# Optimization experiments

Hardware: AMD Instinct MI355X
Metric: run time of the kernel (lower is better)

Reference implementation:

```python
import jax, jax.numpy as jnp
import numpy as np

NUM_HEAD = 16
NUM_SEQ = 2048
NUM_FEAT = 1024
HEAD_DIM = NUM_FEAT // NUM_HEAD
LN_EPS = 1e-5


def _constants():
    # decay per head: log(1 - 2^{-5-h})
    decay = jnp.log(1.0 - 2.0 ** (-5.0 - jnp.arange(NUM_HEAD, dtype=jnp.float32)))
    idx = jnp.arange(NUM_SEQ, dtype=jnp.float32)
    diff = idx[:, None] - idx[None, :]                      # [s, s]
    # exp(diff * decay) on lower triangle (incl. diagonal), 0 above
    mask = jnp.where(diff[None] >= 0, jnp.exp(diff[None] * decay[:, None, None]), 0.0)  # [h, s, s]
    # rotary angles: each frequency repeated twice
    angle = 1.0 / 10000.0 ** jnp.linspace(0.0, 1.0, HEAD_DIM // 2)
    angle = jnp.repeat(angle, 2)                            # [hd]
    sin = jnp.sin(idx[:, None] * angle[None, :])            # [s, hd]
    cos = jnp.cos(idx[:, None] * angle[None, :])
    return mask, sin, cos


def _rotate_every_two(x):
    x1 = x[..., ::2]
    x2 = x[..., 1::2]
    return jnp.stack((-x2, x1), axis=-1).reshape(x.shape)


def setup_inputs() -> dict:
    key = jax.random.key(0)
    ks = jax.random.split(key, 5)
    b, s, d = 4, NUM_SEQ, NUM_FEAT
    x = jax.random.normal(ks[0], (b, s, d), dtype=jnp.float32)
    Wq = jax.random.normal(ks[1], (d, d), dtype=jnp.float32) * 0.02
    Wk = jax.random.normal(ks[2], (d, d), dtype=jnp.float32) * 0.02
    Wv = jax.random.normal(ks[3], (d, d), dtype=jnp.float32) * 0.02
    Wo = jax.random.normal(ks[4], (d, d), dtype=jnp.float32) * 0.02
    ln_w = jnp.ones((HEAD_DIM,), dtype=jnp.float32)
    ln_b = jnp.zeros((HEAD_DIM,), dtype=jnp.float32)
    return {"x": x, "Wq": Wq, "Wk": Wk, "Wv": Wv, "Wo": Wo, "ln_w": ln_w, "ln_b": ln_b}


def reference(x, Wq, Wk, Wv, Wo, ln_w, ln_b):
    b, s, d = x.shape
    h, hd = NUM_HEAD, HEAD_DIM
    mask, sin, cos = _constants()

    def proj(W):
        # torch Linear (no bias): x @ W.T -> [b, h, s, hd]
        return (x @ W.T).reshape(b, s, h, hd).transpose(0, 2, 1, 3)

    q, k, v = proj(Wq), proj(Wk), proj(Wv)
    # rotary theta shift (sin/cos broadcast over batch & head)
    q = q * cos + _rotate_every_two(q) * sin
    k = k * cos + _rotate_every_two(k) * sin

    r = jnp.einsum('bhsd,bhtd->bhst', q, k) * mask[None]    # decay-masked scores
    o = jnp.einsum('bhst,bhtd->bhsd', r, v)                 # [b, h, s, hd]

    # LayerNorm over head_dim
    mu = jnp.mean(o, axis=-1, keepdims=True)
    var = jnp.var(o, axis=-1, keepdims=True)
    y = (o - mu) * jax.lax.rsqrt(var + LN_EPS) * ln_w + ln_b

    y = y.transpose(0, 2, 1, 3).reshape(b, s, d)
    return jax.nn.silu(y) @ Wo.T
```

## Files before the change

### kernel.cpp

```cpp
#include <hip/hip_runtime.h>
#include <math.h>

typedef unsigned short u16;
typedef __attribute__((ext_vector_type(8))) short short8;
typedef __attribute__((ext_vector_type(4))) float floatx4;

#define LDS_AS(p) ((__attribute__((address_space(3))) void*)(p))
#define GLB_AS(p) ((const __attribute__((address_space(1))) void*)(p))

__device__ __forceinline__ u16 f2bf(float f) {
  unsigned int u = __float_as_uint(f);
  u += 0x7fffu + ((u >> 16) & 1u);
  return (u16)(u >> 16);
}

__device__ __forceinline__ void gld16(const void* g, void* l) {
  __builtin_amdgcn_global_load_lds(GLB_AS(g), LDS_AS(l), 16, 0, 0);
}

__device__ __forceinline__ floatx4 mfma16(short8 a, short8 b, floatx4 c) {
  return __builtin_amdgcn_mfma_f32_16x16x32_bf16(a, b, c, 0, 0, 0);
}


__global__ void prep_kernel(const float* __restrict__ x, const float* __restrict__ Wq,
                            const float* __restrict__ Wk, const float* __restrict__ Wv,
                            const float* __restrict__ Wo, u16* __restrict__ xp,
                            u16* __restrict__ wqkvp, u16* __restrict__ wop,
                            float2* __restrict__ rtab) {
  int i = blockIdx.x * blockDim.x + threadIdx.x;
  const int str = gridDim.x * blockDim.x;
  for (; i < 3211264; i += str) {
    if (i < 3145728) {
      int U; u16* d;
      const float* s;
      if (i < 2097152)      { U = i;           d = xp;    s = x;  }
      else if (i < 2883584) { U = i - 2097152; d = wqkvp; s = nullptr; }
      else                  { U = i - 2883584; d = wop;   s = Wo; }
      const int tile = U >> 12;
      const int kc   = (U >> 7) & 31;
      const int lane = (U >> 1) & 63;
      const int jh   = U & 1;
      const int scol = kc * 32 + (lane >> 4) * 8 + jh * 4;
      int srow = tile * 16 + (lane & 15);
      if (s == nullptr) {
        const int sel = srow >> 10;
        srow &= 1023;
        s = (sel == 0) ? Wq : (sel == 1) ? Wk : Wv;
      }
      float4 v = ((const float4*)s)[srow * 256 + (scol >> 2)];
      ushort4 o;
      o.x = f2bf(v.x); o.y = f2bf(v.y); o.z = f2bf(v.z); o.w = f2bf(v.w);
      ((ushort4*)d)[U] = o;
    } else {
      const int t = i - 3145728;
      const int seq = t >> 5, dh = t & 31;
      const float freq = exp2f(-(float)dh * 0.42863594770f);
      float sn, cs;
      __sincosf((float)seq * freq, &sn, &cs);
      rtab[t] = make_float2(sn, cs);
    }
  }
}

template <int EPI>
__global__ __launch_bounds__(256, 2)
void gemm_bt(const u16* __restrict__ A, const u16* __restrict__ Bw, int K,
             u16* __restrict__ qb, u16* __restrict__ kb, u16* __restrict__ vtb,
             u16* __restrict__ kwt, const float2* __restrict__ rtab,
             float* __restrict__ outp) {
  constexpr int AP   = (EPI == 0) ? 8 : 4;
  constexpr int BUFU = (AP + 16) * 512;
  constexpr int AOFF = AP * 512;
  constexpr int AI   = (EPI == 0) ? 8 : 4;
  constexpr int IH   = (EPI == 0) ? 2 : 1;
  __shared__ __align__(16) u16 smem[3 * 12288];
  const int tid = threadIdx.x;
  const int w = tid >> 6, lane = tid & 63;
  const int quad = lane >> 4, l15 = lane & 15;
  const int m0 = blockIdx.y * (EPI == 0 ? 128 : 64), n0 = blockIdx.x * 256;

  const size_t tsz = (size_t)(K >> 5) * 512;
  const u16* A0 = A + ((size_t)(m0 >> 4) + (EPI == 0 ? 2 * w : w)) * tsz + lane * 8;
  const u16* A1 = A0 + tsz;
  const u16* Bb = Bw + ((size_t)(n0 >> 4) + 4 * w) * tsz + lane * 8;

  auto stage = [&](int buf, int kc) {
    const int nb = buf * BUFU;
    gld16(A0 + (size_t)kc * 512, &smem[nb + (EPI == 0 ? 2 * w : w) * 512]);
    if constexpr (EPI == 0)
      gld16(A1 + (size_t)kc * 512, &smem[nb + (2 * w + 1) * 512]);
#pragma unroll
    for (int e = 0; e < 4; ++e)
      gld16(Bb + (size_t)e * tsz + (size_t)kc * 512,
            &smem[nb + AOFF + (4 * w + e) * 512]);
  };

  floatx4 acc[AI][4] = {};
  const int NT = K >> 5;

  stage(0, 0);
  stage(1, 1);
  if constexpr (EPI == 0)
    asm volatile("s_waitcnt vmcnt(6)" ::: "memory");
  else
    asm volatile("s_waitcnt vmcnt(5)" ::: "memory");
  __builtin_amdgcn_s_barrier();

  int cur = 0, stg = 2;
  for (int t = 0; t < NT; ++t) {
    const u16* Ap = &smem[cur * BUFU];
    const u16* Bp = Ap + AOFF;
    short8 a[AI], b[4];
#pragma unroll
    for (int i = 0; i < AI; ++i)
      a[i] = *(const short8*)&Ap[i * 512 + lane * 8];
#pragma unroll
    for (int j = 0; j < 4; ++j)
      b[j] = *(const short8*)&Bp[(w * 4 + j) * 512 + lane * 8];
    if (t + 2 < NT) {
      stage(stg, t + 2);
      if constexpr (EPI == 0)
        asm volatile("s_waitcnt vmcnt(6)" ::: "memory");
      else
        asm volatile("s_waitcnt vmcnt(5)" ::: "memory");
    } else {
      asm volatile("s_waitcnt vmcnt(0)" ::: "memory");
    }
    __builtin_amdgcn_s_barrier();
    asm volatile("s_waitcnt lgkmcnt(0)" ::: "memory");
    __builtin_amdgcn_sched_barrier(0);
    __builtin_amdgcn_s_setprio(1);
#pragma unroll
    for (int i = 0; i < AI; ++i)
#pragma unroll
      for (int j = 0; j < 4; ++j)
        acc[i][j] = mfma16(a[i], b[j], acc[i][j]);
    __builtin_amdgcn_s_setprio(0);
    asm volatile("" ::: "memory");
    __builtin_amdgcn_s_barrier();
    asm volatile("" ::: "memory");
    cur = (cur == 2) ? 0 : cur + 1;
    stg = (stg == 2) ? 0 : stg + 1;
  }

  u16* scr = &smem[w * 4096];

  const int ncb = n0 + w * 64;

#pragma unroll
  for (int ih = 0; ih < IH; ++ih) {
    const int mrb = m0 + ih * 64;

    if (EPI == 0) {
      const int which = n0 >> 10;
      const int c1024 = ncb & 1023;
      const int bidx = mrb >> 11;
      const int hh = c1024 >> 6;
      const int seq0 = mrb & 2047;
      const int chk = seq0 >> 7;

      if (which < 2) {
#pragma unroll
        for (int j = 0; j < 4; ++j) {
          const int d = j * 16 + l15;
          const int dc = d >> 3, dl = d & 7;
#pragma unroll
          for (int i = 0; i < 4; ++i)
#pragma unroll
            for (int r = 0; r < 4; ++r) {
              const int sl = i * 16 + quad * 4 + r;
              const int seq = seq0 + sl;
              const float v = acc[ih * 4 + i][j][r];
              const float p = __shfl_xor(v, 1, 64);
              const float2 sc = rtab[(d >> 1) + seq * 32];
              const float res = (d & 1) ? (v * sc.y + p * sc.x) : (v * sc.y - p * sc.x);
              scr[sl * 64 + (((dc + (sl >> 2)) & 7) << 3) + dl] = f2bf(res);
            }
        }
        u16* dst = ((which == 0) ? qb : kb) +
                   (((size_t)(bidx * 16 + hh) * 16 + chk) << 13);
#pragma unroll
        for (int nl = 0; nl < 4; ++nl)
#pragma unroll
          for (int kk2 = 0; kk2 < 2; ++kk2) {
            const int slr = nl * 16 + l15;
            const int slot = ((kk2 * 4 + quad) + (slr >> 2)) & 7;
            short8 vv = *(const short8*)&scr[slr * 64 + slot * 8];
            *(short8*)(dst + (((ih * 4 + nl) * 2 + kk2) * 512) + lane * 8) = vv;
          }
        if (which == 1) {
          const float l2h = __log2f(1.0f - exp2f(-(float)(5 + hh)));
#pragma unroll
          for (int j = 0; j < 4; ++j) {
            const int d = j * 16 + l15;
#pragma unroll
            for (int i = 0; i < 4; ++i) {
              ushort4 pk;
#pragma unroll
              for (int r = 0; r < 4; ++r) {
                const int sl = i * 16 + quad * 4 + r;
                const int seq = seq0 + sl;
                const float v = acc[ih * 4 + i][j][r];
                const float p = __shfl_xor(v, 1, 64);
                const float2 sc = rtab[(d >> 1) + seq * 32];
                const float res = (d & 1) ? (v * sc.y + p * sc.x) : (v * sc.y - p * sc.x);
                const float wgt = exp2f((float)(127 - (seq & 127)) * l2h);
                ((u16*)&pk)[r] = f2bf(res * wgt);
              }
              *(ushort4*)&scr[d * 64 + ((i * 16 + quad * 4 + 8 * (d & 7)) & 63)] = pk;
            }
          }
          u16* dw = kwt + (((size_t)(bidx * 16 + hh) * 16 + chk) << 13);
#pragma unroll
          for (int m = 0; m < 4; ++m)
#pragma unroll
            for (int ks2 = 0; ks2 < 2; ++ks2) {
              const int dr = m * 16 + l15;
              const int col = ((ks2 * 32 + quad * 8) + 8 * (dr & 7)) & 63;
              short8 vv = *(const short8*)&scr[dr * 64 + col];
              *(short8*)(dw + ((m * 4 + ih * 2 + ks2) * 512) + lane * 8) = vv;
            }
        }
      } else {
#pragma unroll
        for (int j = 0; j < 4; ++j) {
          const int d = j * 16 + l15;
#pragma unroll
          for (int i = 0; i < 4; ++i) {
            ushort4 pk;
            pk.x = f2bf(acc[ih * 4 + i][j][0]);
            pk.y = f2bf(acc[ih * 4 + i][j][1]);
            pk.z = f2bf(acc[ih * 4 + i][j][2]);
            pk.w = f2bf(acc[ih * 4 + i][j][3]);
            *(ushort4*)&scr[d * 64 + ((i * 16 + quad * 4 + 8 * (d & 7)) & 63)] = pk;
          }
        }
        u16* dh = vtb + (((size_t)(bidx * 16 + hh) * 16 + chk) << 13);
#pragma unroll
        for (int m = 0; m < 4; ++m)
#pragma unroll
          for (int ks2 = 0; ks2 < 2; ++ks2) {
            const int dr = m * 16 + l15;
            const int col = ((ks2 * 32 + quad * 8) + 8 * (dr & 7)) & 63;
            short8 vv = *(const short8*)&scr[dr * 64 + col];
            *(short8*)(dh + ((m * 4 + ih * 2 + ks2) * 512) + lane * 8) = vv;
          }
      }
    } else {
      float* scrf = (float*)scr;
      const int lr4 = lane >> 4, lc16 = lane & 15;
#pragma unroll
      for (int p = 0; p < 4; ++p) {
#pragma unroll
        for (int j = 0; j < 4; ++j)
#pragma unroll
          for (int r = 0; r < 4; ++r)
            scrf[(quad * 4 + r) * 65 + j * 16 + l15] = acc[p][j][r];
#pragma unroll
        for (int cch = 0; cch < 4; ++cch) {
          const int rr = cch * 4 + lr4;
          float4 vv = *(const float4*)&scrf[rr * 65 + lc16 * 4];
          *(float4*)&outp[(size_t)(mrb + p * 16 + rr) * 1024 + ncb + lc16 * 4] = vv;
        }
      }
    }
  }
}

__global__ __launch_bounds__(256, 4)
void kvchunk_kernel(const u16* __restrict__ kwt, const u16* __restrict__ vtb,
                    float* __restrict__ U) {
  __shared__ __align__(16) u16 kls[16 * 512];
  __shared__ __align__(16) u16 vls[16 * 512];
  const int c = blockIdx.x, bh = blockIdx.y;
  const int tid = threadIdx.x, w = tid >> 6, lane = tid & 63;
  const int quad = lane >> 4, l15 = lane & 15;
  const u16* kg = kwt + (((size_t)bh * 16 + c) << 13);
  const u16* vg = vtb + (((size_t)bh * 16 + c) << 13);
#pragma unroll
  for (int rg = 0; rg < 4; ++rg) {
    const int rid = w * 4 + rg;
    gld16(kg + rid * 512 + lane * 8, &kls[rid * 512]);
    gld16(vg + rid * 512 + lane * 8, &vls[rid * 512]);
  }
  __syncthreads();
  floatx4 acc[4] = {};
#pragma unroll
  for (int kst = 0; kst < 4; ++kst) {
    short8 bf = *(const short8*)&vls[(w * 4 + kst) * 512 + lane * 8];
#pragma unroll
    for (int m = 0; m < 4; ++m) {
      short8 af = *(const short8*)&kls[(m * 4 + kst) * 512 + lane * 8];
      acc[m] = mfma16(af, bf, acc[m]);
    }
  }
  float* Ub = U + ((size_t)bh * 16 + c) * 4096;
#pragma unroll
  for (int m = 0; m < 4; ++m)
#pragma unroll
    for (int r = 0; r < 4; ++r)
      Ub[(m * 16 + quad * 4 + r) * 64 + w * 16 + l15] = acc[m][r];
}

__global__ void scan_kernel(const float* __restrict__ U, u16* __restrict__ Sb) {
  const int bh = blockIdx.x;
  const int w = threadIdx.x >> 6, l = threadIdx.x & 63;
  const int h = bh & 15;
  const float l2 = __log2f(1.0f - exp2f(-(float)(5 + h)));
  const float lamL = exp2f(128.0f * l2);
  float S[16];
#pragma unroll
  for (int i = 0; i < 16; ++i) S[i] = 0.f;
  for (int c = 0; c < 16; ++c) {
    u16* sp = Sb + (((size_t)bh * 16 + c) << 12);
#pragma unroll
    for (int g = 0; g < 2; ++g) {
      short8 pk;
#pragma unroll
      for (int j = 0; j < 8; ++j) ((u16*)&pk)[j] = f2bf(S[g * 8 + j]);
      const int lp = ((w & 1) * 2 + g) * 16 + (l & 15);
      *(short8*)(sp + (((l >> 4) * 2 + (w >> 1)) * 512) + lp * 8) = pk;
    }
    const float* up = U + ((size_t)bh * 16 + c) * 4096 + (w * 16) * 64 + l;
#pragma unroll
    for (int dk = 0; dk < 16; ++dk)
      S[dk] = lamL * S[dk] + up[dk * 64];
  }
}

__global__ __launch_bounds__(256, 2)
void attn_chunk_kernel(const u16* __restrict__ qb, const u16* __restrict__ kb,
                       const u16* __restrict__ vtb, const u16* __restrict__ Sb,
                       const float* __restrict__ lnw, const float* __restrict__ lnb,
                       u16* __restrict__ yb) {
  __shared__ __align__(16) u16 kls[16 * 512];
  __shared__ __align__(16) u16 vls[16 * 512];
  __shared__ __align__(16) u16 Sls[8 * 512];
  __shared__ __align__(16) u16 pls[4 * 32 * 40];

  const int c = blockIdx.x, bh = blockIdx.y, h = bh & 15;
  const int tid = threadIdx.x;
  const int w = tid >> 6, lane = tid & 63, quad = lane >> 4, l15 = lane & 15;
  const float l2 = __log2f(1.0f - exp2f(-(float)(5 + h)));

  const u16* kg = kb + (((size_t)bh * 16 + c) << 13);
  const u16* vg = vtb + (((size_t)bh * 16 + c) << 13);
  const u16* Sg = Sb + (((size_t)bh * 16 + c) << 12);
#pragma unroll
  for (int rg = 0; rg < 4; ++rg) {
    const int kid = w * 4 + rg;
    gld16(kg + kid * 512 + lane * 8, &kls[kid * 512]);
    gld16(vg + kid * 512 + lane * 8, &vls[kid * 512]);
  }
#pragma unroll
  for (int e = 0; e < 2; ++e) {
    const int rid = w * 2 + e;
    gld16(Sg + rid * 512 + lane * 8, &Sls[rid * 512]);
  }

  short8 qf[2][2];
  {
    const u16* qp = qb + (((size_t)bh * 16 + c) << 13);
#pragma unroll
    for (int i = 0; i < 2; ++i)
#pragma unroll
      for (int kk = 0; kk < 2; ++kk)
        qf[i][kk] = *(const short8*)(qp + (((w * 2 + i) * 2 + kk) * 512) + lane * 8);
  }
  float lnwv[4], lnbv[4];
#pragma unroll
  for (int jd = 0; jd < 4; ++jd) {
    lnwv[jd] = lnw[jd * 16 + l15];
    lnbv[jd] = lnb[jd * 16 + l15];
  }
  __syncthreads();

  floatx4 sacc[2][8] = {};
#pragma unroll
  for (int kk = 0; kk < 2; ++kk) {
    short8 bf[8];
#pragma unroll
    for (int j = 0; j < 8; ++j)
      bf[j] = *(const short8*)&kls[(j * 2 + kk) * 512 + lane * 8];
#pragma unroll
    for (int i = 0; i < 2; ++i)
#pragma unroll
      for (int j = 0; j < 8; ++j)
        sacc[i][j] = mfma16(qf[i][kk], bf[j], sacc[i][j]);
  }

  floatx4 oacc[2][4] = {};
#pragma unroll
  for (int kk = 0; kk < 2; ++kk)
#pragma unroll
    for (int nd = 0; nd < 4; ++nd) {
      short8 sf = *(const short8*)&Sls[(nd * 2 + kk) * 512 + lane * 8];
#pragma unroll
      for (int i = 0; i < 2; ++i)
        oacc[i][nd] = mfma16(qf[i][kk], sf, oacc[i][nd]);
    }
  float rowf[8];
#pragma unroll
  for (int i = 0; i < 2; ++i)
#pragma unroll
    for (int r = 0; r < 4; ++r)
      rowf[i * 4 + r] = exp2f((float)(w * 32 + i * 16 + quad * 4 + r) * l2);
  const float lam1 = exp2f(l2);
#pragma unroll
  for (int i = 0; i < 2; ++i)
#pragma unroll
    for (int nd = 0; nd < 4; ++nd)
#pragma unroll
      for (int r = 0; r < 4; ++r)
        oacc[i][nd][r] *= rowf[i * 4 + r] * lam1;

  float colf[8];
#pragma unroll
  for (int j = 0; j < 8; ++j) colf[j] = exp2f(-(float)(j * 16 + l15) * l2);
  u16* pw = &pls[w * 1280];
#pragma unroll
  for (int kst = 0; kst < 4; ++kst) {
#pragma unroll
    for (int jl = 0; jl < 2; ++jl) {
      const int j = kst * 2 + jl;
#pragma unroll
      for (int i = 0; i < 2; ++i)
#pragma unroll
        for (int r = 0; r < 4; ++r) {
          const int srow = i * 16 + quad * 4 + r;
          const int dlt = (w * 32 + srow) - (j * 16 + l15);
          const float v =
              (dlt >= 0) ? sacc[i][j][r] * rowf[i * 4 + r] * colf[j] : 0.0f;
          pw[srow * 40 + jl * 16 + l15] = f2bf(v);
        }
    }
    short8 pf[2], vf[4];
#pragma unroll
    for (int i = 0; i < 2; ++i)
      pf[i] = *(const short8*)&pw[(i * 16 + l15) * 40 + quad * 8];
#pragma unroll
    for (int jd = 0; jd < 4; ++jd)
      vf[jd] = *(const short8*)&vls[(jd * 4 + kst) * 512 + lane * 8];
#pragma unroll
    for (int i = 0; i < 2; ++i)
#pragma unroll
      for (int jd = 0; jd < 4; ++jd)
        oacc[i][jd] = mfma16(pf[i], vf[jd], oacc[i][jd]);
  }

  __syncthreads();
  u16* scrw = &kls[w * 2048];
  const int b = bh >> 4;
#pragma unroll
  for (int i = 0; i < 2; ++i)
#pragma unroll
    for (int r = 0; r < 4; ++r) {
      float sum = 0.f, ssq = 0.f;
#pragma unroll
      for (int jd = 0; jd < 4; ++jd) {
        const float v = oacc[i][jd][r];
        sum += v;
        ssq += v * v;
      }
#pragma unroll
      for (int off = 1; off < 16; off <<= 1) {
        sum += __shfl_xor(sum, off, 64);
        ssq += __shfl_xor(ssq, off, 64);
      }
      const float mu = sum * (1.0f / 64.0f);
      const float var = ssq * (1.0f / 64.0f) - mu * mu;
      const float rst = rsqrtf(var + 1e-5f);
      const int sl = i * 16 + quad * 4 + r;
#pragma unroll
      for (int jd = 0; jd < 4; ++jd) {
        const float z = (oacc[i][jd][r] - mu) * rst * lnwv[jd] + lnbv[jd];
        const float y = z / (1.0f + expf(-z));
        const int f = jd * 16 + l15;
        scrw[sl * 64 + ((((f >> 3) + (sl >> 2)) & 7) << 3) + (f & 7)] = f2bf(y);
      }
    }
  const int tile0 = b * 128 + c * 8 + w * 2;
#pragma unroll
  for (int tt = 0; tt < 2; ++tt)
#pragma unroll
    for (int kcl = 0; kcl < 2; ++kcl) {
      const int row = tt * 16 + l15;
      const int slot = ((kcl * 4 + quad) + (row >> 2)) & 7;
      short8 vv = *(const short8*)&scrw[row * 64 + slot * 8];
      *(short8*)(yb + ((size_t)(tile0 + tt) * 32 + h * 2 + kcl) * 512 + lane * 8) = vv;
    }
}

extern "C" void kernel_launch(void* const* d_in, const int* in_sizes, int n_in,
                              void* d_out, int out_size, void* d_ws, size_t ws_size,
                              hipStream_t stream) {
  const float* x   = (const float*)d_in[0];
  const float* Wq  = (const float*)d_in[1];
  const float* Wk  = (const float*)d_in[2];
  const float* Wv  = (const float*)d_in[3];
  const float* Wo  = (const float*)d_in[4];
  const float* lnw = (const float*)d_in[5];
  const float* lnb = (const float*)d_in[6];
  float* out = (float*)d_out;

  char* ws = (char*)d_ws;
  u16* xbf  = (u16*)(ws + 0);
  u16* wqkv = (u16*)(ws + 16777216);
  u16* Sb   = (u16*)(ws + 16777216);
  u16* qbuf = (u16*)(ws + 25165824);
  u16* kbuf = (u16*)(ws + 41943040);
  u16* vtb  = (u16*)(ws + 58720256);
  u16* wo   = (u16*)(ws + 75497472);
  float2* rtab = (float2*)(ws + 77594624);
  u16* yb   = xbf;
  u16* kwt  = (u16*)d_out;
  float* Ubuf = (float*)((char*)d_out + 16777216);

  prep_kernel<<<dim3(1024), dim3(256), 0, stream>>>(x, Wq, Wk, Wv, Wo, xbf, wqkv, wo,
                                                    rtab);
  gemm_bt<0><<<dim3(12, 64), dim3(256), 0, stream>>>(xbf, wqkv, 1024, qbuf, kbuf, vtb,
                                                     kwt, rtab, nullptr);
  kvchunk_kernel<<<dim3(16, 64), dim3(256), 0, stream>>>(kwt, vtb, Ubuf);
  scan_kernel<<<dim3(64), dim3(256), 0, stream>>>(Ubuf, Sb);
  attn_chunk_kernel<<<dim3(16, 64), dim3(256), 0, stream>>>(qbuf, kbuf, vtb, Sb, lnw,
                                                            lnb, yb);
  gemm_bt<1><<<dim3(4, 128), dim3(256), 0, stream>>>(yb, wo, 1024, nullptr, nullptr,
                                                     nullptr, nullptr, nullptr, out);
}
```

Before: 243.4 us.

## Fuse per-chunk KV outer products with the decay scan into one pipelined kernel

```diff
diff --git a/kernel.cpp b/kernel.cpp
--- a/kernel.cpp
+++ b/kernel.cpp
@@ -268,64 +268,76 @@
   }
 }
 
-__global__ __launch_bounds__(256, 4)
-void kvchunk_kernel(const u16* __restrict__ kwt, const u16* __restrict__ vtb,
-                    float* __restrict__ U) {
-  __shared__ __align__(16) u16 kls[16 * 512];
-  __shared__ __align__(16) u16 vls[16 * 512];
-  const int c = blockIdx.x, bh = blockIdx.y;
+__global__ __launch_bounds__(256, 2)
+void kvscan_kernel(const u16* __restrict__ kwt, const u16* __restrict__ vtb,
+                   u16* __restrict__ Sb) {
+  __shared__ __align__(16) u16 kls[2][16 * 512];
+  __shared__ __align__(16) u16 vls[2][16 * 512];
+  const int bh = blockIdx.x;
   const int tid = threadIdx.x, w = tid >> 6, lane = tid & 63;
   const int quad = lane >> 4, l15 = lane & 15;
-  const u16* kg = kwt + (((size_t)bh * 16 + c) << 13);
-  const u16* vg = vtb + (((size_t)bh * 16 + c) << 13);
-#pragma unroll
-  for (int rg = 0; rg < 4; ++rg) {
-    const int rid = w * 4 + rg;
-    gld16(kg + rid * 512 + lane * 8, &kls[rid * 512]);
-    gld16(vg + rid * 512 + lane * 8, &vls[rid * 512]);
-  }
-  __syncthreads();
-  floatx4 acc[4] = {};
-#pragma unroll
-  for (int kst = 0; kst < 4; ++kst) {
-    short8 bf = *(const short8*)&vls[(w * 4 + kst) * 512 + lane * 8];
-#pragma unroll
-    for (int m = 0; m < 4; ++m) {
-      short8 af = *(const short8*)&kls[(m * 4 + kst) * 512 + lane * 8];
-      acc[m] = mfma16(af, bf, acc[m]);
-    }
-  }
-  float* Ub = U + ((size_t)bh * 16 + c) * 4096;
-#pragma unroll
-  for (int m = 0; m < 4; ++m)
-#pragma unroll
-    for (int r = 0; r < 4; ++r)
-      Ub[(m * 16 + quad * 4 + r) * 64 + w * 16 + l15] = acc[m][r];
-}
-
-__global__ void scan_kernel(const float* __restrict__ U, u16* __restrict__ Sb) {
-  const int bh = blockIdx.x;
-  const int w = threadIdx.x >> 6, l = threadIdx.x & 63;
   const int h = bh & 15;
   const float l2 = __log2f(1.0f - exp2f(-(float)(5 + h)));
   const float lamL = exp2f(128.0f * l2);
-  float S[16];
-#pragma unroll
-  for (int i = 0; i < 16; ++i) S[i] = 0.f;
+
+  const u16* kg = kwt + ((size_t)bh << 17);
+  const u16* vg = vtb + ((size_t)bh << 17);
+  u16* sbase = Sb + ((size_t)bh << 16);
+
+  auto stage = [&](int buf, int c) {
+    const u16* kc = kg + ((size_t)c << 13);
+    const u16* vc = vg + ((size_t)c << 13);
+#pragma unroll
+    for (int rg = 0; rg < 4; ++rg) {
+      const int rid = w * 4 + rg;
+      gld16(kc + rid * 512 + lane * 8, &kls[buf][rid * 512]);
+      gld16(vc + rid * 512 + lane * 8, &vls[buf][rid * 512]);
+    }
+  };
+
+  float S[4][4] = {};
+
+  stage(0, 0);
+  int buf = 0;
   for (int c = 0; c < 16; ++c) {
-    u16* sp = Sb + (((size_t)bh * 16 + c) << 12);
-#pragma unroll
-    for (int g = 0; g < 2; ++g) {
-      short8 pk;
-#pragma unroll
-      for (int j = 0; j < 8; ++j) ((u16*)&pk)[j] = f2bf(S[g * 8 + j]);
-      const int lp = ((w & 1) * 2 + g) * 16 + (l & 15);
-      *(short8*)(sp + (((l >> 4) * 2 + (w >> 1)) * 512) + lp * 8) = pk;
-    }
-    const float* up = U + ((size_t)bh * 16 + c) * 4096 + (w * 16) * 64 + l;
-#pragma unroll
-    for (int dk = 0; dk < 16; ++dk)
-      S[dk] = lamL * S[dk] + up[dk * 64];
+    if (c + 1 < 16) {
+      stage(buf ^ 1, c + 1);
+      asm volatile("s_waitcnt vmcnt(8)" ::: "memory");
+    } else {
+      asm volatile("s_waitcnt vmcnt(0)" ::: "memory");
+    }
+    __builtin_amdgcn_s_barrier();
+    asm volatile("" ::: "memory");
+
+    u16* sp = sbase + ((size_t)c << 12);
+#pragma unroll
+    for (int m = 0; m < 4; ++m) {
+      ushort4 pk;
+#pragma unroll
+      for (int r = 0; r < 4; ++r) ((u16*)&pk)[r] = f2bf(S[m][r]);
+      const int lanep = ((m & 1) * 2 + (quad >> 1)) * 16 + l15;
+      *(ushort4*)(sp + (w * 2 + (m >> 1)) * 512 + lanep * 8 + (quad & 1) * 4) = pk;
+    }
+
+    floatx4 acc[4] = {};
+#pragma unroll
+    for (int kst = 0; kst < 4; ++kst) {
+      short8 bf = *(const short8*)&vls[buf][(w * 4 + kst) * 512 + lane * 8];
+#pragma unroll
+      for (int m = 0; m < 4; ++m) {
+        short8 af = *(const short8*)&kls[buf][(m * 4 + kst) * 512 + lane * 8];
+        acc[m] = mfma16(af, bf, acc[m]);
+      }
+    }
+#pragma unroll
+    for (int m = 0; m < 4; ++m)
+#pragma unroll
+      for (int r = 0; r < 4; ++r)
+        S[m][r] = lamL * S[m][r] + acc[m][r];
+
+    asm volatile("" ::: "memory");
+    __builtin_amdgcn_s_barrier();
+    buf ^= 1;
   }
 }
 
@@ -515,14 +527,12 @@
   float2* rtab = (float2*)(ws + 77594624);
   u16* yb   = xbf;
   u16* kwt  = (u16*)d_out;
-  float* Ubuf = (float*)((char*)d_out + 16777216);
 
   prep_kernel<<<dim3(1024), dim3(256), 0, stream>>>(x, Wq, Wk, Wv, Wo, xbf, wqkv, wo,
                                                     rtab);
   gemm_bt<0><<<dim3(12, 64), dim3(256), 0, stream>>>(xbf, wqkv, 1024, qbuf, kbuf, vtb,
                                                      kwt, rtab, nullptr);
-  kvchunk_kernel<<<dim3(16, 64), dim3(256), 0, stream>>>(kwt, vtb, Ubuf);
-  scan_kernel<<<dim3(64), dim3(256), 0, stream>>>(Ubuf, Sb);
+  kvscan_kernel<<<dim3(64), dim3(256), 0, stream>>>(kwt, vtb, Sb);
   attn_chunk_kernel<<<dim3(16, 64), dim3(256), 0, stream>>>(qbuf, kbuf, vtb, Sb, lnw,
                                                             lnb, yb);
   gemm_bt<1><<<dim3(4, 128), dim3(256), 0, stream>>>(yb, wo, 1024, nullptr, nullptr,
```

New measurement: 236.3 us. -2.9%, faster.
